# Performance work log

Hardware: AMD Instinct MI355X
Metric: run time of the kernel (lower is better)

## Reference

```python
import jax, jax.numpy as jnp
import numpy as np

B_PARAM = 1.0
BAND_WIDTH = 0.5
LOSS_WEIGHT = 1.0
EPS_REL = 1e-5
EPS_NORM = 1e-12


def setup_inputs() -> dict:
    key = jax.random.key(0)
    k1, k2 = jax.random.split(key)
    images = jax.random.normal(k1, (1, 256, 96, 96), dtype=jnp.float32)
    gt = jax.random.normal(k2, (1, 256, 96, 96), dtype=jnp.float32)
    return {"images": images, "gt": gt}


def _cosine_raw_distance(i_feat, t_feat):
    # _create_using_dot_p: center both by mean of t over (n, h, w), L2-normalize
    # along channels, then pairwise dot products -> cosine distance in [0, 1].
    mean_t = jnp.mean(t_feat, axis=(0, 2, 3), keepdims=True)
    i_c = i_feat - mean_t
    t_c = t_feat - mean_t
    i_n = i_c / jnp.maximum(jnp.sqrt(jnp.sum(i_c * i_c, axis=1, keepdims=True)), EPS_NORM)
    t_n = t_c / jnp.maximum(jnp.sqrt(jnp.sum(t_c * t_c, axis=1, keepdims=True)), EPS_NORM)
    n, c, h, w = i_n.shape
    t_v = t_n.reshape(n, c, h * w)
    # dot[n, h, w, s] = sum_c i_n[n,c,h,w] * t_v[n,c,s]   (the conv2d 1x1 kernel trick)
    dot = jnp.einsum('nchw,ncs->nhws', i_n, t_v)
    dist = jnp.clip((1.0 - dot) / 2.0, 0.0, None)
    return dist  # [n, h, w, h*w]


def _cx_loss(i_feat, t_feat):
    raw = _cosine_raw_distance(i_feat, t_feat)                      # [n,h,w,s]
    # relative distance (Eq. 2): divide each row by its min over target positions
    rel = raw / (jnp.min(raw, axis=-1, keepdims=True) + EPS_REL)
    w = jnp.exp((B_PARAM - rel) / BAND_WIDTH)
    cx = w / jnp.sum(w, axis=-1, keepdims=True)                     # row softmax-like
    max_gt_sim = jnp.max(cx, axis=(1, 2))                           # [n, s]
    cs = jnp.mean(max_gt_sim, axis=1)                               # [n]
    loss = jnp.mean(-jnp.log(cs))
    return loss * LOSS_WEIGHT


def reference(images, gt):
    # use_vgg=False, crop_quarter=False, h*w <= max_1d_size**2 -> direct CX loss.
    return _cx_loss(images, gt)
```

## Files before the change

### kernel.cpp

```cpp
#include <hip/hip_runtime.h>
#include <hip/hip_bf16.h>

#define S 9216
#define C 256
#define NCT 6
#define NG  (NCT*8)
#define SCH 1152

typedef __bf16 bf16x8 __attribute__((ext_vector_type(8)));
typedef float f32x4 __attribute__((ext_vector_type(4)));
typedef unsigned short us8 __attribute__((ext_vector_type(8)));
typedef unsigned short us4 __attribute__((ext_vector_type(4)));

#define GLOAD_LDS16(g, l) __builtin_amdgcn_global_load_lds( \
    (const __attribute__((address_space(1))) void*)(g),     \
    (__attribute__((address_space(3))) void*)(l), 16, 0, 0)

#define A2C 2.8853900817779268f

__device__ __forceinline__ float bf2f(unsigned short u) {
    return __uint_as_float(((unsigned)u) << 16);
}
__device__ __forceinline__ unsigned short f2bfbits(float x) {
    __hip_bfloat16 h = __float2bfloat16(x);
    return *reinterpret_cast<unsigned short*>(&h);
}

__global__ __launch_bounds__(256) void k_mean(const float* __restrict__ gt,
                                              float* __restrict__ meanT) {
    const int c = blockIdx.x;
    const float* p = gt + (size_t)c * S;
    float s = 0.f;
    for (int i = threadIdx.x; i < S; i += 256) s += p[i];
    for (int m = 1; m < 64; m <<= 1) s += __shfl_xor(s, m, 64);
    __shared__ float red[4];
    if ((threadIdx.x & 63) == 0) red[threadIdx.x >> 6] = s;
    __syncthreads();
    if (threadIdx.x == 0)
        meanT[c] = (red[0] + red[1] + red[2] + red[3]) * (1.0f / S);
}

__global__ __launch_bounds__(256) void k_ssq(const float* __restrict__ img,
                                             const float* __restrict__ gt,
                                             const float* __restrict__ meanT,
                                             float* __restrict__ ssqP,
                                             float* __restrict__ rowmin,
                                             float* __restrict__ rowsum,
                                             float* __restrict__ colmaxLog) {
    __shared__ float sm[16];
    const int part = blockIdx.x & 15;
    const int sb   = blockIdx.x >> 4;
    const int t    = threadIdx.x;
    if (t < 16) sm[t] = meanT[part * 16 + t];
    const int s = sb * 256 + t;
    if (part == 0) {
        rowmin[s]    = __uint_as_float(0x7f800000u);
        rowsum[s]    = 0.f;
        colmaxLog[s] = 0.f;
    }
    __syncthreads();
    float si = 0.f, st = 0.f;
    #pragma unroll 8
    for (int k = 0; k < 16; ++k) {
        const int c = part * 16 + k;
        const float m  = sm[k];
        const float di = img[(size_t)c * S + s] - m;
        const float dt = gt [(size_t)c * S + s] - m;
        si += di * di;
        st += dt * dt;
    }
    ssqP[(size_t)part * S + s]        = si;
    ssqP[(size_t)(part + 16) * S + s] = st;
}

__global__ __launch_bounds__(256) void k_write(const float* __restrict__ img,
                                               const float* __restrict__ gt,
                                               const float* __restrict__ meanT,
                                               const float* __restrict__ ssqP,
                                               __hip_bfloat16* __restrict__ A,
                                               __hip_bfloat16* __restrict__ B) {
    __shared__ float sm[16];
    const int part = blockIdx.x & 15;
    const int sb   = blockIdx.x >> 4;
    const int t    = threadIdx.x;
    if (t < 16) sm[t] = meanT[part * 16 + t];
    __syncthreads();
    const int s = sb * 256 + t;
    float si = 0.f, st = 0.f;
    #pragma unroll
    for (int p = 0; p < 16; ++p) {
        si += ssqP[(size_t)p * S + s];
        st += ssqP[(size_t)(p + 16) * S + s];
    }
    const float ri = 1.0f / fmaxf(sqrtf(si), 1e-12f);
    const float rt = 1.0f / fmaxf(sqrtf(st), 1e-12f);
    const int c0 = part * 16;
    #pragma unroll
    for (int cc = 0; cc < 2; ++cc) {
        us8 va, vb;
        #pragma unroll
        for (int e = 0; e < 8; ++e) {
            const int c = c0 + cc * 8 + e;
            const float m = sm[cc * 8 + e];
            va[e] = f2bfbits((img[(size_t)c * S + s] - m) * ri);
            vb[e] = f2bfbits((gt [(size_t)c * S + s] - m) * rt);
        }
        *reinterpret_cast<us8*>(A + (size_t)s * C + c0 + cc * 8) = va;
        *reinterpret_cast<us8*>(B + (size_t)s * C + c0 + cc * 8) = vb;
    }
}

__global__ __launch_bounds__(256, 3) void k_gemm_store(const __hip_bfloat16* __restrict__ A,
                                                       const __hip_bfloat16* __restrict__ B,
                                                       float* __restrict__ rowmin,
                                                       __hip_bfloat16* __restrict__ Q) {
    __shared__ alignas(16) __hip_bfloat16 As[64 * 256];
    __shared__ alignas(16) __hip_bfloat16 Bs[4 * 2 * 2048];
    const int tid  = threadIdx.x;
    const int lane = tid & 63;
    const int wid  = tid >> 6;
    const int orig = blockIdx.x;
    const int xcd  = orig & 7;
    const int q    = orig >> 3;
    const int colGroup = q / 18;
    const int strip    = xcd * 18 + (q % 18);
    const int rowBase = strip * 64;
    const int cb0     = colGroup * 1536;

    const int frow = lane & 15;
    const int kgrp = lane >> 4;

    {
        const int arow_lo = lane >> 5;
        const int achunk  = lane & 31;
        #pragma unroll
        for (int j = 0; j < 8; ++j) {
            const int row = wid * 16 + j * 2 + arow_lo;
            const int cc  = achunk ^ (row & 7);
            GLOAD_LDS16(A + (size_t)(rowBase + row) * C + cc * 8,
                        &As[(wid * 16 + j * 2) * 256 + lane * 8]);
        }
    }
    const int bcol4  = lane >> 2;
    const int bchunk = (lane & 3) ^ ((lane >> 3) & 3);
    __hip_bfloat16* const BsW = &Bs[wid * 4096];
    const __hip_bfloat16* const Bsrc = B + (size_t)(cb0 + wid * 64) * C;

#define STAGE_B(tt, kk, bb) do {                                              \
    _Pragma("unroll")                                                         \
    for (int i_ = 0; i_ < 4; ++i_) {                                          \
        GLOAD_LDS16(Bsrc + (size_t)((tt) * 256 + i_ * 16 + bcol4) * C         \
                         + (kk) * 32 + bchunk * 8,                            \
                    &BsW[(bb) * 2048 + i_ * 512]);                            \
    } } while (0)

    STAGE_B(0, 0, 0);
    STAGE_B(0, 1, 1);

    asm volatile("s_waitcnt vmcnt(4)" ::: "memory");
    __builtin_amdgcn_s_barrier();

    const int bswz = (kgrp ^ ((frow >> 1) & 3)) * 8;

    float vmin[4][4];
    #pragma unroll
    for (int m = 0; m < 4; ++m)
        #pragma unroll
        for (int qq = 0; qq < 4; ++qq) vmin[m][qq] = 1e30f;

    for (int t = 0; t < NCT; ++t) {
        f32x4 acc[4][4] = {};
        #pragma unroll
        for (int kt = 0; kt < 8; ++kt) {
            if (t > 0 && kt < 2)               asm volatile("s_waitcnt vmcnt(20)" ::: "memory");
            else if (t == NCT - 1 && kt == 7)  asm volatile("s_waitcnt vmcnt(0)"  ::: "memory");
            else                               asm volatile("s_waitcnt vmcnt(4)"  ::: "memory");

            const int bufc = kt & 1;

            bf16x8 af[4], bfr[4];
            #pragma unroll
            for (int m = 0; m < 4; ++m) {
                const int row = m * 16 + frow;
                const int p   = (kt * 4 + kgrp) ^ (frow & 7);
                af[m] = *reinterpret_cast<const bf16x8*>(&As[row * 256 + p * 8]);
            }
            #pragma unroll
            for (int n = 0; n < 4; ++n)
                bfr[n] = *reinterpret_cast<const bf16x8*>(
                    &BsW[bufc * 2048 + (n * 16 + frow) * 32 + bswz]);

            asm volatile("s_waitcnt lgkmcnt(0)" ::: "memory");
            __builtin_amdgcn_sched_barrier(0);

            if (kt <= 5) {
                STAGE_B(t, kt + 2, bufc);
            } else if (t + 1 < NCT) {
                STAGE_B(t + 1, kt - 6, bufc);
            }

            #pragma unroll
            for (int m = 0; m < 4; ++m)
                #pragma unroll
                for (int n = 0; n < 4; ++n)
                    acc[m][n] = __builtin_amdgcn_mfma_f32_16x16x32_bf16(af[m], bfr[n], acc[m][n], 0, 0, 0);
        }

        const int colBase = cb0 + t * 256;
        #pragma unroll
        for (int n = 0; n < 4; ++n) {
            const int cg = colBase + wid * 64 + n * 16 + frow;
            #pragma unroll
            for (int m = 0; m < 4; ++m) {
                us4 pk;
                #pragma unroll
                for (int qq = 0; qq < 4; ++qq) {
                    const float raw = fmaxf(0.5f * (1.0f - acc[m][n][qq]), 0.0f);
                    vmin[m][qq] = fminf(vmin[m][qq], raw);
                    pk[qq] = f2bfbits(raw);
                }
                *reinterpret_cast<us4*>(Q + (size_t)cg * S + rowBase + m * 16 + kgrp * 4) = pk;
            }
        }
    }
#undef STAGE_B

    #pragma unroll
    for (int m = 0; m < 4; ++m)
        #pragma unroll
        for (int qq = 0; qq < 4; ++qq) {
            float v = vmin[m][qq];
            v = fminf(v, __shfl_xor(v, 1, 64));
            v = fminf(v, __shfl_xor(v, 2, 64));
            v = fminf(v, __shfl_xor(v, 4, 64));
            v = fminf(v, __shfl_xor(v, 8, 64));
            if (frow == 0)
                atomicMin((unsigned int*)&rowmin[rowBase + m * 16 + kgrp * 4 + qq],
                          __float_as_uint(v));
        }
}

__global__ __launch_bounds__(256) void k_rowsum(const __hip_bfloat16* __restrict__ Q,
                                                const float* __restrict__ rowmin,
                                                float* __restrict__ rowsum) {
    __shared__ float sBrN[64];
    __shared__ float srs[64];
    const int t  = threadIdx.x;
    const int r0 = (blockIdx.x >> 3) * 64;
    const int s0 = (blockIdx.x & 7) * SCH;
    if (t < 64) {
        sBrN[t] = -A2C / (rowmin[r0 + t] + 1e-5f);
        srs[t]  = 0.f;
    }
    __syncthreads();
    const int roct = (t & 7) * 8;
    const int ss   = t >> 3;
    float brn[8];
    #pragma unroll
    for (int j = 0; j < 8; ++j) brn[j] = sBrN[roct + j];
    const __hip_bfloat16* base = Q + r0 + roct;

    float sums[8] = {};
    #pragma unroll 4
    for (int i = 0; i < SCH / 32; ++i) {
        const int s = s0 + ss + i * 32;
        const us8 v = *reinterpret_cast<const us8*>(base + (size_t)s * S);
        #pragma unroll
        for (int j = 0; j < 8; ++j)
            sums[j] += exp2f(fmaf(brn[j], bf2f(v[j]), A2C));
    }
    #pragma unroll
    for (int j = 0; j < 8; ++j) {
        float x = sums[j];
        x += __shfl_xor(x, 8, 64);
        x += __shfl_xor(x, 16, 64);
        x += __shfl_xor(x, 32, 64);
        if ((t & 63) < 8) atomicAdd(&srs[roct + j], x);
    }
    __syncthreads();
    if (t < 64) atomicAdd(&rowsum[r0 + t], srs[t]);
}

__global__ __launch_bounds__(256) void k_colmax(const __hip_bfloat16* __restrict__ Q,
                                                const float* __restrict__ rowmin,
                                                const float* __restrict__ rowsum,
                                                float* __restrict__ colmaxLog) {
    __shared__ float sBrN[64];
    __shared__ float sCA[64];
    const int t  = threadIdx.x;
    const int r0 = (blockIdx.x >> 3) * 64;
    const int s0 = (blockIdx.x & 7) * SCH;
    if (t < 64) {
        sBrN[t] = -A2C / (rowmin[r0 + t] + 1e-5f);
        sCA[t]  = A2C + 64.0f - __log2f(rowsum[r0 + t]);
    }
    __syncthreads();
    const int roct = (t & 7) * 8;
    const int ss   = t >> 3;
    float brn[8], ca[8];
    #pragma unroll
    for (int j = 0; j < 8; ++j) { brn[j] = sBrN[roct + j]; ca[j] = sCA[roct + j]; }
    const __hip_bfloat16* base = Q + r0 + roct;

    #pragma unroll 4
    for (int i = 0; i < SCH / 32; ++i) {
        const int s = s0 + ss + i * 32;
        const us8 v = *reinterpret_cast<const us8*>(base + (size_t)s * S);
        float mx = -1e30f;
        #pragma unroll
        for (int j = 0; j < 8; ++j)
            mx = fmaxf(mx, fmaf(brn[j], bf2f(v[j]), ca[j]));
        mx = fmaxf(mx, __shfl_xor(mx, 1, 64));
        mx = fmaxf(mx, __shfl_xor(mx, 2, 64));
        mx = fmaxf(mx, __shfl_xor(mx, 4, 64));
        if ((t & 7) == 0)
            atomicMax((unsigned int*)&colmaxLog[s], __float_as_uint(fmaxf(mx, 0.0f)));
    }
}

__global__ __launch_bounds__(256) void k_final(const float* __restrict__ colmaxLog,
                                               float* __restrict__ out) {
    float s = 0.f;
    for (int i = threadIdx.x; i < S; i += 256) s += exp2f(colmaxLog[i]);
    for (int m = 1; m < 64; m <<= 1) s += __shfl_xor(s, m, 64);
    __shared__ float red[4];
    if ((threadIdx.x & 63) == 0) red[threadIdx.x >> 6] = s;
    __syncthreads();
    if (threadIdx.x == 0) {
        const float total = red[0] + red[1] + red[2] + red[3];
        out[0] = -logf(total * (5.421010862427522e-20f / (float)S));
    }
}

extern "C" void kernel_launch(void* const* d_in, const int* in_sizes, int n_in,
                              void* d_out, int out_size, void* d_ws, size_t ws_size,
                              hipStream_t stream) {
    const float* img = (const float*)d_in[0];
    const float* gt  = (const float*)d_in[1];

    float* ws        = (float*)d_ws;
    float* meanT     = ws;
    float* rowmin    = ws + 256;
    float* rowsum    = rowmin + S;
    float* colmaxLog = rowsum + S;
    __hip_bfloat16* A = (__hip_bfloat16*)(colmaxLog + S);
    __hip_bfloat16* B = A + (size_t)S * C;
    __hip_bfloat16* Q = B + (size_t)S * C;
    float* ssqP = (float*)Q;
    float* out = (float*)d_out;

    k_mean <<<C, 256, 0, stream>>>(gt, meanT);
    k_ssq  <<<576, 256, 0, stream>>>(img, gt, meanT, ssqP, rowmin, rowsum, colmaxLog);
    k_write<<<576, 256, 0, stream>>>(img, gt, meanT, ssqP, A, B);

    k_gemm_store<<<864, 256, 0, stream>>>(A, B, rowmin, Q);
    k_rowsum<<<1152, 256, 0, stream>>>(Q, rowmin, rowsum);
    k_colmax<<<1152, 256, 0, stream>>>(Q, rowmin, rowsum, colmaxLog);

    k_final<<<1, 256, 0, stream>>>(colmaxLog, out);
}
```

Before: 212.9 us.

## Write centered bf16 in ssq pass, normalize in place; retune grids and occupancy

The sum-of-squares kernel now also writes the mean-centered bf16 values of A and B, so the second pass only reads bf16 back and scales by the inverse norm instead of re-reading both fp32 inputs. This removes one fp32 read of both inputs but adds a bf16 read-modify-write and a second bf16 rounding step, which slightly changes precision. The rowsum and colmax kernels are split into twice as many smaller blocks (SCH halved, unroll reduced), and the GEMM's launch_bounds minimum occupancy drops from 3 to 2 blocks per CU.

```diff
diff --git a/kernel.cpp b/kernel.cpp
--- a/kernel.cpp
+++ b/kernel.cpp
@@ -5,7 +5,7 @@
 #define C 256
 #define NCT 6
 #define NG  (NCT*8)
-#define SCH 1152
+#define SCH 576
 
 typedef __bf16 bf16x8 __attribute__((ext_vector_type(8)));
 typedef float f32x4 __attribute__((ext_vector_type(4)));
@@ -44,6 +44,8 @@
                                              const float* __restrict__ gt,
                                              const float* __restrict__ meanT,
                                              float* __restrict__ ssqP,
+                                             __hip_bfloat16* __restrict__ A,
+                                             __hip_bfloat16* __restrict__ B,
                                              float* __restrict__ rowmin,
                                              float* __restrict__ rowsum,
                                              float* __restrict__ colmaxLog) {
@@ -59,33 +61,35 @@
         colmaxLog[s] = 0.f;
     }
     __syncthreads();
+    const int c0 = part * 16;
     float si = 0.f, st = 0.f;
-    #pragma unroll 8
-    for (int k = 0; k < 16; ++k) {
-        const int c = part * 16 + k;
-        const float m  = sm[k];
-        const float di = img[(size_t)c * S + s] - m;
-        const float dt = gt [(size_t)c * S + s] - m;
-        si += di * di;
-        st += dt * dt;
+    #pragma unroll
+    for (int cc = 0; cc < 2; ++cc) {
+        us8 va, vb;
+        #pragma unroll
+        for (int e = 0; e < 8; ++e) {
+            const int c = c0 + cc * 8 + e;
+            const float m  = sm[cc * 8 + e];
+            const float di = img[(size_t)c * S + s] - m;
+            const float dt = gt [(size_t)c * S + s] - m;
+            si += di * di;
+            st += dt * dt;
+            va[e] = f2bfbits(di);
+            vb[e] = f2bfbits(dt);
+        }
+        *reinterpret_cast<us8*>(A + (size_t)s * C + c0 + cc * 8) = va;
+        *reinterpret_cast<us8*>(B + (size_t)s * C + c0 + cc * 8) = vb;
     }
     ssqP[(size_t)part * S + s]        = si;
     ssqP[(size_t)(part + 16) * S + s] = st;
 }
 
-__global__ __launch_bounds__(256) void k_write(const float* __restrict__ img,
-                                               const float* __restrict__ gt,
-                                               const float* __restrict__ meanT,
-                                               const float* __restrict__ ssqP,
-                                               __hip_bfloat16* __restrict__ A,
-                                               __hip_bfloat16* __restrict__ B) {
-    __shared__ float sm[16];
+__global__ __launch_bounds__(256) void k_norm(const float* __restrict__ ssqP,
+                                              __hip_bfloat16* __restrict__ A,
+                                              __hip_bfloat16* __restrict__ B) {
     const int part = blockIdx.x & 15;
     const int sb   = blockIdx.x >> 4;
-    const int t    = threadIdx.x;
-    if (t < 16) sm[t] = meanT[part * 16 + t];
-    __syncthreads();
-    const int s = sb * 256 + t;
+    const int s    = sb * 256 + threadIdx.x;
     float si = 0.f, st = 0.f;
     #pragma unroll
     for (int p = 0; p < 16; ++p) {
@@ -97,20 +101,19 @@
     const int c0 = part * 16;
     #pragma unroll
     for (int cc = 0; cc < 2; ++cc) {
-        us8 va, vb;
+        us8 va = *reinterpret_cast<const us8*>(A + (size_t)s * C + c0 + cc * 8);
+        us8 vb = *reinterpret_cast<const us8*>(B + (size_t)s * C + c0 + cc * 8);
         #pragma unroll
         for (int e = 0; e < 8; ++e) {
-            const int c = c0 + cc * 8 + e;
-            const float m = sm[cc * 8 + e];
-            va[e] = f2bfbits((img[(size_t)c * S + s] - m) * ri);
-            vb[e] = f2bfbits((gt [(size_t)c * S + s] - m) * rt);
+            va[e] = f2bfbits(bf2f(va[e]) * ri);
+            vb[e] = f2bfbits(bf2f(vb[e]) * rt);
         }
         *reinterpret_cast<us8*>(A + (size_t)s * C + c0 + cc * 8) = va;
         *reinterpret_cast<us8*>(B + (size_t)s * C + c0 + cc * 8) = vb;
     }
 }
 
-__global__ __launch_bounds__(256, 3) void k_gemm_store(const __hip_bfloat16* __restrict__ A,
+__global__ __launch_bounds__(256, 2) void k_gemm_store(const __hip_bfloat16* __restrict__ A,
                                                        const __hip_bfloat16* __restrict__ B,
                                                        float* __restrict__ rowmin,
                                                        __hip_bfloat16* __restrict__ Q) {
@@ -246,8 +249,8 @@
     __shared__ float sBrN[64];
     __shared__ float srs[64];
     const int t  = threadIdx.x;
-    const int r0 = (blockIdx.x >> 3) * 64;
-    const int s0 = (blockIdx.x & 7) * SCH;
+    const int r0 = (blockIdx.x >> 4) * 64;
+    const int s0 = (blockIdx.x & 15) * SCH;
     if (t < 64) {
         sBrN[t] = -A2C / (rowmin[r0 + t] + 1e-5f);
         srs[t]  = 0.f;
@@ -261,7 +264,7 @@
     const __hip_bfloat16* base = Q + r0 + roct;
 
     float sums[8] = {};
-    #pragma unroll 4
+    #pragma unroll 2
     for (int i = 0; i < SCH / 32; ++i) {
         const int s = s0 + ss + i * 32;
         const us8 v = *reinterpret_cast<const us8*>(base + (size_t)s * S);
@@ -288,8 +291,8 @@
     __shared__ float sBrN[64];
     __shared__ float sCA[64];
     const int t  = threadIdx.x;
-    const int r0 = (blockIdx.x >> 3) * 64;
-    const int s0 = (blockIdx.x & 7) * SCH;
+    const int r0 = (blockIdx.x >> 4) * 64;
+    const int s0 = (blockIdx.x & 15) * SCH;
     if (t < 64) {
         sBrN[t] = -A2C / (rowmin[r0 + t] + 1e-5f);
         sCA[t]  = A2C + 64.0f - __log2f(rowsum[r0 + t]);
@@ -302,7 +305,7 @@
     for (int j = 0; j < 8; ++j) { brn[j] = sBrN[roct + j]; ca[j] = sCA[roct + j]; }
     const __hip_bfloat16* base = Q + r0 + roct;
 
-    #pragma unroll 4
+    #pragma unroll 2
     for (int i = 0; i < SCH / 32; ++i) {
         const int s = s0 + ss + i * 32;
         const us8 v = *reinterpret_cast<const us8*>(base + (size_t)s * S);
@@ -349,13 +352,14 @@
     float* ssqP = (float*)Q;
     float* out = (float*)d_out;
 
-    k_mean <<<C, 256, 0, stream>>>(gt, meanT);
-    k_ssq  <<<576, 256, 0, stream>>>(img, gt, meanT, ssqP, rowmin, rowsum, colmaxLog);
-    k_write<<<576, 256, 0, stream>>>(img, gt, meanT, ssqP, A, B);
+    k_mean<<<C, 256, 0, stream>>>(gt, meanT);
+    k_ssq <<<576, 256, 0, stream>>>(img, gt, meanT, ssqP, A, B,
+                                    rowmin, rowsum, colmaxLog);
+    k_norm<<<576, 256, 0, stream>>>(ssqP, A, B);
 
     k_gemm_store<<<864, 256, 0, stream>>>(A, B, rowmin, Q);
-    k_rowsum<<<1152, 256, 0, stream>>>(Q, rowmin, rowsum);
-    k_colmax<<<1152, 256, 0, stream>>>(Q, rowmin, rowsum, colmaxLog);
+    k_rowsum<<<2304, 256, 0, stream>>>(Q, rowmin, rowsum);
+    k_colmax<<<2304, 256, 0, stream>>>(Q, rowmin, rowsum, colmaxLog);
 
     k_final<<<1, 256, 0, stream>>>(colmaxLog, out);
 }
```

Measured after the change: 221.4 us. 4.0% more time.
